# Kernel optimization log

Measured on AMD Instinct MI355X. Metric: run time of the kernel, lower is better.

Reference implementation:

```python
import jax, jax.numpy as jnp
import numpy as np

HEADS = 4
AGENT = 49  # 7x7 agent tokens
LN_EPS = 1e-5


def setup_inputs() -> dict:
    key = jax.random.key(0)
    ks = jax.random.split(key, 3)
    B, C, H, W = 2, 128, 56, 56
    x = jax.random.normal(ks[0], (B, C, H, W), jnp.float32)
    # 1x1 convs == per-pixel linear maps; store as [out_ch, in_ch]
    w_qkv = jax.random.normal(ks[1], (3 * C, C), jnp.float32) * (C ** -0.5)
    w_proj = jax.random.normal(ks[2], (C, C), jnp.float32) * (C ** -0.5)
    b_proj = jnp.zeros((C,), jnp.float32)
    ln_g = jnp.ones((C,), jnp.float32)
    ln_b = jnp.zeros((C,), jnp.float32)
    return {"x": x, "w_qkv": w_qkv, "w_proj": w_proj, "b_proj": b_proj,
            "ln_g": ln_g, "ln_b": ln_b}


def reference(x, w_qkv, w_proj, b_proj, ln_g, ln_b):
    B, C, H, W = x.shape
    heads = HEADS
    hd = C // heads
    N = H * W
    scale = hd ** -0.5
    a = int(AGENT ** 0.5)  # 7; H,W divisible by a -> exact adaptive avg pool

    # 1x1-conv QKV: [B,3C,H,W] -> [B,3,heads,hd,N] -> q,k,v [B,h,N,hd]
    qkv = jnp.einsum('oc,bchw->bohw', w_qkv, x).reshape(B, 3, heads, hd, N)
    q = jnp.transpose(qkv[:, 0], (0, 1, 3, 2))
    k = jnp.transpose(qkv[:, 1], (0, 1, 3, 2))
    v = jnp.transpose(qkv[:, 2], (0, 1, 3, 2))

    # agent tokens: adaptive avg pool to (a,a) == uniform block mean
    agent = x.reshape(B, C, a, H // a, a, W // a).mean(axis=(3, 5))  # [B,C,a,a]
    agent = agent.reshape(B, heads, hd, AGENT)
    agent = jnp.transpose(agent, (0, 1, 3, 2))  # [B,h,A,hd]

    # stage 1: compress q through agent tokens
    q_to_agent = jax.nn.softmax(
        jnp.einsum('bhnd,bhad->bhna', q * scale, agent), axis=-1)  # [B,h,N,A]
    q_compressed = jnp.einsum('bhna,bhad->bhnd', q_to_agent, agent)  # [B,h,N,hd]

    # stage 2: full N x N attention with compressed queries
    attn = jax.nn.softmax(
        jnp.einsum('bhnd,bhmd->bhnm', q_compressed * scale, k), axis=-1)
    out = jnp.einsum('bhnm,bhmd->bhnd', attn, v)  # [B,h,N,hd]

    # merge heads -> [B,N,C], 1x1-conv proj, LayerNorm over C
    out = jnp.transpose(out, (0, 2, 1, 3)).reshape(B, N, C)
    out = jnp.einsum('bnc,oc->bno', out, w_proj) + b_proj
    mu = out.mean(-1, keepdims=True)
    var = out.var(-1, keepdims=True)
    out = (out - mu) / jnp.sqrt(var + LN_EPS) * ln_g + ln_b
    return jnp.transpose(out.reshape(B, H, W, C), (0, 3, 1, 2))
```

## Files before the change

### kernel.cpp

```cpp
#include <hip/hip_runtime.h>
#include <hip/hip_bf16.h>
#include <stdint.h>

typedef unsigned short u16;
typedef __attribute__((ext_vector_type(8))) short short8;
typedef __attribute__((ext_vector_type(4))) short short4v;
typedef __attribute__((ext_vector_type(4))) float f32x4;

#define NB 2
#define NC 128
#define NHD 4
#define HD 32
#define NN 3136
#define NA 49
#define NSPLIT 4
#define NKP 3200
#define NTILE 25
#define SCALE 0.17677669529663687f
#define LOG2E 1.4426950408889634f
#define QSC (SCALE * LOG2E)

__device__ inline u16 bfb(float f) {
    __hip_bfloat16 h = __float2bfloat16(f);
    return *(u16*)&h;
}
__device__ inline float b2f(u16 w) {
    return __uint_as_float(((uint32_t)w) << 16);
}
__device__ inline short4v pack4(float a, float b, float c, float d) {
    union { short4v s; __hip_bfloat162 h[2]; } u;
    u.h[0] = __float22bfloat162_rn(make_float2(a, b));
    u.h[1] = __float22bfloat162_rn(make_float2(c, d));
    return u.s;
}
__device__ inline float ldf(const void* p, size_t i, int f) {
    return f ? b2f(((const u16*)p)[i]) : ((const float*)p)[i];
}
__device__ inline void gld16(const u16* g, u16* l) {
    __builtin_amdgcn_global_load_lds(
        (__attribute__((address_space(1))) void*)(g),
        (__attribute__((address_space(3))) void*)(l), 16, 0, 0);
}
__device__ inline void stage8k(const u16* g, u16* lds, int w, int lane) {
    gld16(g + (size_t)(w * 64 + lane) * 8,       lds + (size_t)w * 512);
    gld16(g + (size_t)(256 + w * 64 + lane) * 8, lds + 2048 + (size_t)w * 512);
}

__global__ void k_detect(const u16* __restrict__ raw, int* __restrict__ flag) {
    __shared__ int cnt;
    if (threadIdx.x == 0) cnt = 0;
    __syncthreads();
    u16 w = raw[threadIdx.x * 97];
    float f = b2f(w);
    float a = fabsf(f);
    if (a >= 1e-4f && a <= 100.0f) atomicAdd(&cnt, 1);
    __syncthreads();
    if (threadIdx.x == 0) *flag = (cnt >= 230) ? 1 : 0;
}

__global__ __launch_bounds__(256) void k_prep(const void* __restrict__ xr,
                                              const void* __restrict__ wq,
                                              const void* __restrict__ wp,
                                              const void* __restrict__ bp,
                                              const void* __restrict__ g,
                                              const void* __restrict__ bb,
                                              u16* __restrict__ xT,
                                              u16* __restrict__ wbf,
                                              u16* __restrict__ wpb,
                                              float* __restrict__ bgb,
                                              u16* __restrict__ agb,
                                              u16* __restrict__ agT,
                                              const int* __restrict__ flag) {
    __shared__ u16 tile[128][18];
    int bx = blockIdx.x, t = threadIdx.x;
    int f = *flag;
    if (bx < 392) {
        int b = bx / 196;
        int n0 = (bx % 196) * 16;
        int c = t >> 1, nh = (t & 1) * 8;
        size_t src = ((size_t)(b * 128 + c)) * NN + n0 + nh;
#pragma unroll
        for (int i = 0; i < 8; ++i) tile[c][nh + i] = bfb(ldf(xr, src + i, f));
        __syncthreads();
        int n = t >> 4, c0 = (t & 15) * 8;
        short8 o;
#pragma unroll
        for (int i = 0; i < 8; ++i) o[i] = (short)tile[c0 + i][n];
        *(short8*)&xT[((size_t)b * NN + n0 + n) * 128 + c0] = o;
    } else if (bx < 584) {
        int i = (bx - 392) * 256 + t;
        wbf[i] = bfb(ldf(wq, i, f));
    } else if (bx < 648) {
        int i = (bx - 584) * 256 + t;
        wpb[i] = bfb(ldf(wp, i, f));
    } else if (bx < 650) {
        int i = (bx - 648) * 256 + t;
        if (i < 128)      bgb[i] = ldf(bp, i, f);
        else if (i < 256) bgb[i] = ldf(g, i - 128, f);
        else if (i < 384) bgb[i] = ldf(bb, i - 256, f);
    } else {
        int idx = (bx - 650) * 256 + t;
        const int NPOOL = NB * NC * NA;
        if (idx < NPOOL) {
            int b = idx / (NC * NA);
            int r = idx % (NC * NA);
            int c = r / NA;
            int a = r % NA;
            int ai = a / 7, aj = a % 7;
            size_t base = ((size_t)(b * NC + c)) * NN + ai * 8 * 56 + aj * 8;
            float s = 0.f;
            if (f) {
                const u16* xp = (const u16*)xr + base;
#pragma unroll
                for (int uu = 0; uu < 8; ++uu) {
                    ushort4 a0 = *(const ushort4*)&xp[uu * 56];
                    ushort4 a1 = *(const ushort4*)&xp[uu * 56 + 4];
                    s += b2f(a0.x) + b2f(a0.y) + b2f(a0.z) + b2f(a0.w)
                       + b2f(a1.x) + b2f(a1.y) + b2f(a1.z) + b2f(a1.w);
                }
            } else {
                const float* xp = (const float*)xr + base;
#pragma unroll
                for (int uu = 0; uu < 8; ++uu) {
                    float4 v0 = *(const float4*)&xp[uu * 56];
                    float4 v1 = *(const float4*)&xp[uu * 56 + 4];
                    s += v0.x + v0.y + v0.z + v0.w + v1.x + v1.y + v1.z + v1.w;
                }
            }
            int h = c >> 5, d = c & 31;
            int bh = b * NHD + h;
            u16 val = bfb(s * (1.f / 64.f));
            agb[bh * 2048 + a * 32 + d] = val;
            agT[bh * 2048 + d * 64 + a] = val;
        } else {
            int j = idx - NPOOL;
            if (j < 3840) {
                int bh = j / 480, rem = j % 480;
                int a = 49 + rem / 32, d = rem % 32;
                agb[bh * 2048 + a * 32 + d] = 0;
            } else if (j < 7680) {
                j -= 3840;
                int bh = j / 480, rem = j % 480;
                int a = 49 + rem / 32, d = rem % 32;
                agT[bh * 2048 + d * 64 + a] = 0;
            }
        }
    }
}

__global__ __launch_bounds__(256, 4) void k_qkv2(const u16* __restrict__ xT,
                                                 const u16* __restrict__ wbf,
                                                 u16* __restrict__ qb,
                                                 u16* __restrict__ kbf,
                                                 u16* __restrict__ vtb) {
    int b = blockIdx.z;
    int n0 = blockIdx.x * 64;
    int w = threadIdx.x >> 6, lane = threadIdx.x & 63;
    int c = lane & 15, u = lane >> 4;
    int o0 = blockIdx.y * 64 + w * 16;
    const f32x4 z = {0.f, 0.f, 0.f, 0.f};
    short8 af0 = *(const short8*)&wbf[(o0 + c) * 128 +  0 + u * 8];
    short8 af1 = *(const short8*)&wbf[(o0 + c) * 128 + 32 + u * 8];
    short8 af2 = *(const short8*)&wbf[(o0 + c) * 128 + 64 + u * 8];
    short8 af3 = *(const short8*)&wbf[(o0 + c) * 128 + 96 + u * 8];
    int tq = o0 >> 7, h = (o0 >> 5) & 3, d0 = (o0 & 31) + u * 4;
    size_t bh = (size_t)b * NHD + h;
    const u16* xb = &xT[(size_t)b * NN * 128];
#pragma unroll
    for (int nt = 0; nt < 4; ++nt) {
        int n = n0 + nt * 16 + c;
        f32x4 acc = z;
        acc = __builtin_amdgcn_mfma_f32_16x16x32_bf16(af0,
            *(const short8*)&xb[(size_t)n * 128 +  0 + u * 8], acc, 0, 0, 0);
        acc = __builtin_amdgcn_mfma_f32_16x16x32_bf16(af1,
            *(const short8*)&xb[(size_t)n * 128 + 32 + u * 8], acc, 0, 0, 0);
        acc = __builtin_amdgcn_mfma_f32_16x16x32_bf16(af2,
            *(const short8*)&xb[(size_t)n * 128 + 64 + u * 8], acc, 0, 0, 0);
        acc = __builtin_amdgcn_mfma_f32_16x16x32_bf16(af3,
            *(const short8*)&xb[(size_t)n * 128 + 96 + u * 8], acc, 0, 0, 0);
        if (tq == 0) {
            *(short4v*)&qb[(bh * NN + n) * HD + d0] =
                pack4(acc[0] * QSC, acc[1] * QSC, acc[2] * QSC, acc[3] * QSC);
        } else if (tq == 1) {
            *(short4v*)&kbf[(bh * NKP + n) * HD + d0] =
                pack4(acc[0], acc[1], acc[2], acc[3]);
        } else {
            int tile = n >> 7, kt2 = n & 127;
            int sub = kt2 >> 4, uu = (kt2 >> 2) & 3, jj = n & 3;
            size_t vb0 = ((size_t)bh * NTILE + tile) * 4096 + sub * 512 + uu * 128 + jj;
#pragma unroll
            for (int r = 0; r < 4; ++r)
                vtb[vb0 + (d0 + r) * 4] = bfb(acc[r]);
        }
    }
}

__global__ __launch_bounds__(256, 4) void k_stage1_2(const u16* __restrict__ qb,
                                                     const u16* __restrict__ agb,
                                                     const u16* __restrict__ agT,
                                                     u16* __restrict__ qcb) {
    int b = blockIdx.z, h = blockIdx.y;
    int w = threadIdx.x >> 6, lane = threadIdx.x & 63;
    int c = lane & 15, u = lane >> 4;
    int q0 = blockIdx.x * 64 + w * 16;
    size_t bh = (size_t)b * NHD + h;
    const u16* aB = agb + bh * 2048;
    const u16* aT = agT + bh * 2048;
    const f32x4 z = {0.f, 0.f, 0.f, 0.f};
    short8 qf = *(const short8*)&qb[(bh * NN + q0 + c) * HD + u * 8];
    f32x4 st[4];
#pragma unroll
    for (int t = 0; t < 4; ++t) {
        short8 afr = *(const short8*)&aB[(t * 16 + c) * 32 + u * 8];
        st[t] = __builtin_amdgcn_mfma_f32_16x16x32_bf16(afr, qf, z, 0, 0, 0);
    }
    float e[4][4];
    float lsum = 0.f;
#pragma unroll
    for (int t = 0; t < 4; ++t)
#pragma unroll
        for (int r = 0; r < 4; ++r) {
            float v = __builtin_amdgcn_exp2f(st[t][r]);
            if (t == 3 && !(u == 0 && r == 0)) v = 0.f;
            e[t][r] = v;
            lsum += v;
        }
    lsum += __shfl_xor(lsum, 16);
    lsum += __shfl_xor(lsum, 32);
    float linv = 1.f / lsum;
    f32x4 qlo = z, qhi = z;
#pragma unroll
    for (int t = 0; t < 4; ++t) {
        short4v pf = pack4(e[t][0] * linv, e[t][1] * linv, e[t][2] * linv, e[t][3] * linv);
        short4v alo = *(const short4v*)&aT[c * 64 + t * 16 + u * 4];
        short4v ahi = *(const short4v*)&aT[(c + 16) * 64 + t * 16 + u * 4];
        qlo = __builtin_amdgcn_mfma_f32_16x16x16bf16_1k(alo, pf, qlo, 0, 0, 0);
        qhi = __builtin_amdgcn_mfma_f32_16x16x16bf16_1k(ahi, pf, qhi, 0, 0, 0);
    }
    u16* dst = &qcb[(bh * NN + q0 + c) * HD];
    *(short4v*)&dst[u * 4]      = pack4(qlo[0] * QSC, qlo[1] * QSC, qlo[2] * QSC, qlo[3] * QSC);
    *(short4v*)&dst[16 + u * 4] = pack4(qhi[0] * QSC, qhi[1] * QSC, qhi[2] * QSC, qhi[3] * QSC);
}

__global__ __launch_bounds__(256, 3) void k_flash4(const u16* __restrict__ qc,
                                                   const u16* __restrict__ kb,
                                                   const u16* __restrict__ vt,
                                                   float* __restrict__ op,
                                                   float* __restrict__ lp) {
    __shared__ __align__(16) u16 Ks[2][4096];
    __shared__ __align__(16) u16 Vs[2][4096];
    int b = blockIdx.z;
    int h = blockIdx.y & 3;
    int s = blockIdx.y >> 2;
    int w = threadIdx.x >> 6, lane = threadIdx.x & 63;
    int c = lane & 15, u = lane >> 4;
    int qa = blockIdx.x * 128 + w * 32;
    int qbr = qa + 16;
    if (qa  > NN - 16) qa  = NN - 16;
    if (qbr > NN - 16) qbr = NN - 16;
    size_t bh = (size_t)b * NHD + h;
    const u16* kg = kb + bh * (size_t)NKP * HD;
    const u16* vg = vt + bh * (size_t)NTILE * 4096;
    short8 qfA = *(const short8*)(qc + (bh * NN + qa  + c) * HD + u * 8);
    short8 qfB = *(const short8*)(qc + (bh * NN + qbr + c) * HD + u * 8);
    const f32x4 z = {0.f, 0.f, 0.f, 0.f};
    f32x4 oA0 = z, oA1 = z, oB0 = z, oB1 = z;
    float lA = 0.f, lB = 0.f;
    int t0 = (s * NTILE) / NSPLIT, t1 = ((s + 1) * NTILE) / NSPLIT;
    stage8k(kg + (size_t)t0 * 4096, &Ks[0][0], w, lane);
    stage8k(vg + (size_t)t0 * 4096, &Vs[0][0], w, lane);
#pragma unroll 1
    for (int t = t0; t < t1; ++t) {
        int buf = (t - t0) & 1;
        __syncthreads();
        if (t + 1 < t1) {
            stage8k(kg + (size_t)(t + 1) * 4096, &Ks[buf ^ 1][0], w, lane);
            stage8k(vg + (size_t)(t + 1) * 4096, &Vs[buf ^ 1][0], w, lane);
        }
        const u16* kp = &Ks[buf][0];
        const u16* vp = &Vs[buf][0];
        int kk = t * 128;
        bool tail = (kk + 128 > NN);
#pragma unroll
        for (int sub = 0; sub < 8; ++sub) {
            short8 kf = *(const short8*)(kp + sub * 512 + c * 32 + u * 8);
            f32x4 sA = __builtin_amdgcn_mfma_f32_16x16x32_bf16(kf, qfA, z, 0, 0, 0);
            f32x4 sB = __builtin_amdgcn_mfma_f32_16x16x32_bf16(kf, qfB, z, 0, 0, 0);
            float eA[4], eB[4];
#pragma unroll
            for (int r = 0; r < 4; ++r) {
                eA[r] = __builtin_amdgcn_exp2f(sA[r]);
                eB[r] = __builtin_amdgcn_exp2f(sB[r]);
            }
            if (tail) {
#pragma unroll
                for (int r = 0; r < 4; ++r)
                    if (kk + sub * 16 + u * 4 + r >= NN) { eA[r] = 0.f; eB[r] = 0.f; }
            }
            lA += (eA[0] + eA[1]) + (eA[2] + eA[3]);
            lB += (eB[0] + eB[1]) + (eB[2] + eB[3]);
            short4v pA = pack4(eA[0], eA[1], eA[2], eA[3]);
            short4v pB = pack4(eB[0], eB[1], eB[2], eB[3]);
            short4v va = *(const short4v*)(vp + sub * 512 + u * 128 + c * 4);
            short4v vb = *(const short4v*)(vp + sub * 512 + u * 128 + (c + 16) * 4);
            oA0 = __builtin_amdgcn_mfma_f32_16x16x16bf16_1k(va, pA, oA0, 0, 0, 0);
            oA1 = __builtin_amdgcn_mfma_f32_16x16x16bf16_1k(vb, pA, oA1, 0, 0, 0);
            oB0 = __builtin_amdgcn_mfma_f32_16x16x16bf16_1k(va, pB, oB0, 0, 0, 0);
            oB1 = __builtin_amdgcn_mfma_f32_16x16x16bf16_1k(vb, pB, oB1, 0, 0, 0);
        }
    }
    lA += __shfl_xor(lA, 16); lA += __shfl_xor(lA, 32);
    lB += __shfl_xor(lB, 16); lB += __shfl_xor(lB, 32);
    float* oba = op + (((size_t)(s * NB + b)) * NN + qa + c) * NC + h * HD;
    *(f32x4*)&oba[u * 4]      = oA0;
    *(f32x4*)&oba[16 + u * 4] = oA1;
    float* obb = op + (((size_t)(s * NB + b)) * NN + qbr + c) * NC + h * HD;
    *(f32x4*)&obb[u * 4]      = oB0;
    *(f32x4*)&obb[16 + u * 4] = oB1;
    if (u == 0) {
        lp[(((size_t)(s * NB + b)) * NHD + h) * NN + qa  + c] = lA;
        lp[(((size_t)(s * NB + b)) * NHD + h) * NN + qbr + c] = lB;
    }
}

__global__ __launch_bounds__(256, 4) void k_proj2(const float* __restrict__ op,
                                                  const float* __restrict__ lp,
                                                  const u16* __restrict__ wpb,
                                                  const float* __restrict__ bgb,
                                                  void* __restrict__ out,
                                                  const int* __restrict__ flag) {
    __shared__ u16 Af[16 * 136];
    __shared__ float red1[4][16], red2[4][16];
    int bx = blockIdx.x;
    int b = bx >= 196;
    int n0 = (bx - b * 196) * 16;
    int t = threadIdx.x;
    {
        int row = t >> 4, c8 = (t & 15) * 8;
        int n = n0 + row;
        int hh = c8 >> 5;
        float ls = 0.f;
#pragma unroll
        for (int s = 0; s < NSPLIT; ++s)
            ls += lp[(((size_t)(s * NB + b)) * NHD + hh) * NN + n];
        float inv = 1.f / ls;
        float v[8] = {};
#pragma unroll
        for (int s = 0; s < NSPLIT; ++s) {
            const float* src = &op[(((size_t)(s * NB + b)) * NN + n) * NC + c8];
            float4 x0 = *(const float4*)&src[0];
            float4 x1 = *(const float4*)&src[4];
            v[0] += x0.x; v[1] += x0.y; v[2] += x0.z; v[3] += x0.w;
            v[4] += x1.x; v[5] += x1.y; v[6] += x1.z; v[7] += x1.w;
        }
        u16* dst = &Af[row * 136 + c8];
#pragma unroll
        for (int i = 0; i < 8; i += 2) {
            __hip_bfloat162 p = __float22bfloat162_rn(make_float2(v[i] * inv, v[i + 1] * inv));
            *(uint32_t*)&dst[i] = *(uint32_t*)&p;
        }
    }
    __syncthreads();
    int w = t >> 6, lane = t & 63, c = lane & 15, u = lane >> 4;
    int oA = w * 32 + c, oB = w * 32 + 16 + c;
    const f32x4 z = {0.f, 0.f, 0.f, 0.f};
    f32x4 cA = z, cB = z;
#pragma unroll
    for (int kf = 0; kf < 4; ++kf) {
        short8 a  = *(const short8*)&Af[c * 136 + kf * 32 + u * 8];
        short8 bA = *(const short8*)&wpb[(size_t)oA * 128 + kf * 32 + u * 8];
        short8 bB = *(const short8*)&wpb[(size_t)oB * 128 + kf * 32 + u * 8];
        cA = __builtin_amdgcn_mfma_f32_16x16x32_bf16(a, bA, cA, 0, 0, 0);
        cB = __builtin_amdgcn_mfma_f32_16x16x32_bf16(a, bB, cB, 0, 0, 0);
    }
    float bpA = bgb[oA], bpB = bgb[oB];
    float s1[4], s2[4];
#pragma unroll
    for (int r = 0; r < 4; ++r) {
        cA[r] += bpA; cB[r] += bpB;
        s1[r] = cA[r] + cB[r];
        s2[r] = cA[r] * cA[r] + cB[r] * cB[r];
    }
#pragma unroll
    for (int off = 1; off < 16; off <<= 1)
#pragma unroll
        for (int r = 0; r < 4; ++r) {
            s1[r] += __shfl_xor(s1[r], off);
            s2[r] += __shfl_xor(s2[r], off);
        }
    if (c == 0)
#pragma unroll
        for (int r = 0; r < 4; ++r) {
            red1[w][u * 4 + r] = s1[r];
            red2[w][u * 4 + r] = s2[r];
        }
    __syncthreads();
    float gA = bgb[128 + oA], beA = bgb[256 + oA];
    float gB = bgb[128 + oB], beB = bgb[256 + oB];
    float outA[4], outB[4];
#pragma unroll
    for (int r = 0; r < 4; ++r) {
        int row = u * 4 + r;
        float S1 = (red1[0][row] + red1[1][row]) + (red1[2][row] + red1[3][row]);
        float S2 = (red2[0][row] + red2[1][row]) + (red2[2][row] + red2[3][row]);
        float mu = S1 * (1.f / NC);
        float ex = S2 * (1.f / NC);
        float rstd = rsqrtf(ex - mu * mu + 1e-5f);
        outA[r] = (cA[r] - mu) * rstd * gA + beA;
        outB[r] = (cB[r] - mu) * rstd * gB + beB;
    }
    int n = n0 + u * 4;
    if (*flag) {
        __hip_bfloat16* ob = (__hip_bfloat16*)out;
        ushort4 sA = make_ushort4(bfb(outA[0]), bfb(outA[1]), bfb(outA[2]), bfb(outA[3]));
        ushort4 sB = make_ushort4(bfb(outB[0]), bfb(outB[1]), bfb(outB[2]), bfb(outB[3]));
        *(ushort4*)&ob[((size_t)(b * NC + oA)) * NN + n] = sA;
        *(ushort4*)&ob[((size_t)(b * NC + oB)) * NN + n] = sB;
    } else {
        float* ob = (float*)out;
        *(float4*)&ob[((size_t)(b * NC + oA)) * NN + n] = make_float4(outA[0], outA[1], outA[2], outA[3]);
        *(float4*)&ob[((size_t)(b * NC + oB)) * NN + n] = make_float4(outB[0], outB[1], outB[2], outB[3]);
    }
}

extern "C" void kernel_launch(void* const* d_in, const int* in_sizes, int n_in,
                              void* d_out, int out_size, void* d_ws, size_t ws_size,
                              hipStream_t stream) {
    const void* x_raw  = d_in[0];
    const void* wq_raw = d_in[1];
    const void* wp_raw = d_in[2];
    const void* bp_raw = d_in[3];
    const void* lg_raw = d_in[4];
    const void* lb_raw = d_in[5];

    float* ws   = (float*)d_ws;
    int*   flag = (int*)d_ws;
    float* bgb  = ws + 16;
    float* op   = bgb + 512;
    float* lp   = op + (size_t)NSPLIT * NB * NN * NC;
    u16*   xT   = (u16*)(lp + (size_t)NSPLIT * NB * NHD * NN);
    u16*   wbf  = xT + (size_t)NB * NN * NC;
    u16*   wpb  = wbf + 3 * NC * NC;
    u16*   qb   = wpb + NC * NC;
    u16*   kbf  = qb + (size_t)NB * NHD * NN * HD;
    u16*   vtb  = kbf + (size_t)NB * NHD * NKP * HD;
    u16*   qcb  = vtb + (size_t)NB * NHD * NTILE * 4096;
    u16*   agb  = qcb + (size_t)NB * NHD * NN * HD;
    u16*   agT  = agb + NB * NHD * 64 * 32;

    k_detect<<<1, 256, 0, stream>>>((const u16*)x_raw, flag);
    k_prep<<<729, 256, 0, stream>>>(x_raw, wq_raw, wp_raw, bp_raw, lg_raw, lb_raw,
                                    xT, wbf, wpb, bgb, agb, agT, flag);
    k_qkv2<<<dim3(NN / 64, 6, NB), 256, 0, stream>>>(xT, wbf, qb, kbf, vtb);
    k_stage1_2<<<dim3(NN / 64, NHD, NB), 256, 0, stream>>>(qb, agb, agT, qcb);
    k_flash4<<<dim3(25, NHD * NSPLIT, NB), 256, 0, stream>>>(qcb, kbf, vtb, op, lp);
    k_proj2<<<392, 256, 0, stream>>>(op, lp, wpb, bgb, d_out, flag);
}
```

Measured before the change: 124.0 us.

## Fuse detect into prep, stage1 into QKV, and store flash partials as bf16

Each prep block now runs the dtype detection itself, which removes the separate detect launch. The agent-compression stage now runs inside the QKV kernel on a Q tile kept in shared memory, so Q is never written to or read back from global memory and one more launch goes away. Flash partial outputs are normalised and stored as bf16 instead of fp32, which halves the traffic into the projection kernel; that kernel recombines the splits weighted by their sums. The cost is some lost precision in the partials and a serial stage1 tail in only two of the six y-blocks of the QKV grid.

```diff
diff --git a/kernel.cpp b/kernel.cpp
--- a/kernel.cpp
+++ b/kernel.cpp
@@ -45,17 +45,14 @@
     gld16(g + (size_t)(w * 64 + lane) * 8,       lds + (size_t)w * 512);
     gld16(g + (size_t)(256 + w * 64 + lane) * 8, lds + 2048 + (size_t)w * 512);
 }
-
-__global__ void k_detect(const u16* __restrict__ raw, int* __restrict__ flag) {
+__device__ inline int detect_local(const u16* raw, int t) {
     __shared__ int cnt;
-    if (threadIdx.x == 0) cnt = 0;
+    if (t == 0) cnt = 0;
     __syncthreads();
-    u16 w = raw[threadIdx.x * 97];
-    float f = b2f(w);
-    float a = fabsf(f);
+    float a = fabsf(b2f(raw[t * 97]));
     if (a >= 1e-4f && a <= 100.0f) atomicAdd(&cnt, 1);
     __syncthreads();
-    if (threadIdx.x == 0) *flag = (cnt >= 230) ? 1 : 0;
+    return cnt >= 230;
 }
 
 __global__ __launch_bounds__(256) void k_prep(const void* __restrict__ xr,
@@ -70,10 +67,10 @@
                                               float* __restrict__ bgb,
                                               u16* __restrict__ agb,
                                               u16* __restrict__ agT,
-                                              const int* __restrict__ flag) {
+                                              int* __restrict__ flagOut) {
     __shared__ u16 tile[128][18];
     int bx = blockIdx.x, t = threadIdx.x;
-    int f = *flag;
+    int f = detect_local((const u16*)xr, t);
     if (bx < 392) {
         int b = bx / 196;
         int n0 = (bx % 196) * 16;
@@ -98,6 +95,7 @@
         if (i < 128)      bgb[i] = ldf(bp, i, f);
         else if (i < 256) bgb[i] = ldf(g, i - 128, f);
         else if (i < 384) bgb[i] = ldf(bb, i - 256, f);
+        if (bx == 648 && t == 0) *flagOut = f;
     } else {
         int idx = (bx - 650) * 256 + t;
         const int NPOOL = NB * NC * NA;
@@ -148,11 +146,14 @@
     }
 }
 
-__global__ __launch_bounds__(256, 4) void k_qkv2(const u16* __restrict__ xT,
-                                                 const u16* __restrict__ wbf,
-                                                 u16* __restrict__ qb,
-                                                 u16* __restrict__ kbf,
-                                                 u16* __restrict__ vtb) {
+__global__ __launch_bounds__(256, 4) void k_qkv_s1(const u16* __restrict__ xT,
+                                                   const u16* __restrict__ wbf,
+                                                   const u16* __restrict__ agb,
+                                                   const u16* __restrict__ agT,
+                                                   u16* __restrict__ kbf,
+                                                   u16* __restrict__ vtb,
+                                                   u16* __restrict__ qcb) {
+    __shared__ u16 qtile[2 * 64 * 40];
     int b = blockIdx.z;
     int n0 = blockIdx.x * 64;
     int w = threadIdx.x >> 6, lane = threadIdx.x & 63;
@@ -179,7 +180,8 @@
         acc = __builtin_amdgcn_mfma_f32_16x16x32_bf16(af3,
             *(const short8*)&xb[(size_t)n * 128 + 96 + u * 8], acc, 0, 0, 0);
         if (tq == 0) {
-            *(short4v*)&qb[(bh * NN + n) * HD + d0] =
+            int hl = (o0 >> 5) & 1;
+            *(short4v*)&qtile[(hl * 64 + nt * 16 + c) * 40 + d0] =
                 pack4(acc[0] * QSC, acc[1] * QSC, acc[2] * QSC, acc[3] * QSC);
         } else if (tq == 1) {
             *(short4v*)&kbf[(bh * NKP + n) * HD + d0] =
@@ -193,59 +195,57 @@
                 vtb[vb0 + (d0 + r) * 4] = bfb(acc[r]);
         }
     }
-}
-
-__global__ __launch_bounds__(256, 4) void k_stage1_2(const u16* __restrict__ qb,
-                                                     const u16* __restrict__ agb,
-                                                     const u16* __restrict__ agT,
-                                                     u16* __restrict__ qcb) {
-    int b = blockIdx.z, h = blockIdx.y;
-    int w = threadIdx.x >> 6, lane = threadIdx.x & 63;
-    int c = lane & 15, u = lane >> 4;
-    int q0 = blockIdx.x * 64 + w * 16;
-    size_t bh = (size_t)b * NHD + h;
-    const u16* aB = agb + bh * 2048;
-    const u16* aT = agT + bh * 2048;
-    const f32x4 z = {0.f, 0.f, 0.f, 0.f};
-    short8 qf = *(const short8*)&qb[(bh * NN + q0 + c) * HD + u * 8];
-    f32x4 st[4];
-#pragma unroll
-    for (int t = 0; t < 4; ++t) {
-        short8 afr = *(const short8*)&aB[(t * 16 + c) * 32 + u * 8];
-        st[t] = __builtin_amdgcn_mfma_f32_16x16x32_bf16(afr, qf, z, 0, 0, 0);
-    }
-    float e[4][4];
-    float lsum = 0.f;
-#pragma unroll
-    for (int t = 0; t < 4; ++t)
-#pragma unroll
-        for (int r = 0; r < 4; ++r) {
-            float v = __builtin_amdgcn_exp2f(st[t][r]);
-            if (t == 3 && !(u == 0 && r == 0)) v = 0.f;
-            e[t][r] = v;
-            lsum += v;
-        }
-    lsum += __shfl_xor(lsum, 16);
-    lsum += __shfl_xor(lsum, 32);
-    float linv = 1.f / lsum;
-    f32x4 qlo = z, qhi = z;
-#pragma unroll
-    for (int t = 0; t < 4; ++t) {
-        short4v pf = pack4(e[t][0] * linv, e[t][1] * linv, e[t][2] * linv, e[t][3] * linv);
-        short4v alo = *(const short4v*)&aT[c * 64 + t * 16 + u * 4];
-        short4v ahi = *(const short4v*)&aT[(c + 16) * 64 + t * 16 + u * 4];
-        qlo = __builtin_amdgcn_mfma_f32_16x16x16bf16_1k(alo, pf, qlo, 0, 0, 0);
-        qhi = __builtin_amdgcn_mfma_f32_16x16x16bf16_1k(ahi, pf, qhi, 0, 0, 0);
-    }
-    u16* dst = &qcb[(bh * NN + q0 + c) * HD];
-    *(short4v*)&dst[u * 4]      = pack4(qlo[0] * QSC, qlo[1] * QSC, qlo[2] * QSC, qlo[3] * QSC);
-    *(short4v*)&dst[16 + u * 4] = pack4(qhi[0] * QSC, qhi[1] * QSC, qhi[2] * QSC, qhi[3] * QSC);
+    if (blockIdx.y < 2) {
+        __syncthreads();
+#pragma unroll
+        for (int tt = w; tt < 8; tt += 4) {
+            int hl2 = tt >> 2, r0 = (tt & 3) * 16;
+            int hg = blockIdx.y * 2 + hl2;
+            size_t bh2 = (size_t)b * NHD + hg;
+            const u16* aB = agb + bh2 * 2048;
+            const u16* aT = agT + bh2 * 2048;
+            short8 qf = *(const short8*)&qtile[(hl2 * 64 + r0 + c) * 40 + u * 8];
+            f32x4 st[4];
+#pragma unroll
+            for (int t2 = 0; t2 < 4; ++t2) {
+                short8 afr = *(const short8*)&aB[(t2 * 16 + c) * 32 + u * 8];
+                st[t2] = __builtin_amdgcn_mfma_f32_16x16x32_bf16(afr, qf, z, 0, 0, 0);
+            }
+            float e[4][4];
+            float lsum = 0.f;
+#pragma unroll
+            for (int t2 = 0; t2 < 4; ++t2)
+#pragma unroll
+                for (int r = 0; r < 4; ++r) {
+                    float v = __builtin_amdgcn_exp2f(st[t2][r]);
+                    if (t2 == 3 && !(u == 0 && r == 0)) v = 0.f;
+                    e[t2][r] = v;
+                    lsum += v;
+                }
+            lsum += __shfl_xor(lsum, 16);
+            lsum += __shfl_xor(lsum, 32);
+            float linv = 1.f / lsum;
+            f32x4 qlo = z, qhi = z;
+#pragma unroll
+            for (int t2 = 0; t2 < 4; ++t2) {
+                short4v pf = pack4(e[t2][0] * linv, e[t2][1] * linv,
+                                   e[t2][2] * linv, e[t2][3] * linv);
+                short4v alo = *(const short4v*)&aT[c * 64 + t2 * 16 + u * 4];
+                short4v ahi = *(const short4v*)&aT[(c + 16) * 64 + t2 * 16 + u * 4];
+                qlo = __builtin_amdgcn_mfma_f32_16x16x16bf16_1k(alo, pf, qlo, 0, 0, 0);
+                qhi = __builtin_amdgcn_mfma_f32_16x16x16bf16_1k(ahi, pf, qhi, 0, 0, 0);
+            }
+            u16* dst = &qcb[(bh2 * NN + n0 + r0 + c) * HD];
+            *(short4v*)&dst[u * 4]      = pack4(qlo[0] * QSC, qlo[1] * QSC, qlo[2] * QSC, qlo[3] * QSC);
+            *(short4v*)&dst[16 + u * 4] = pack4(qhi[0] * QSC, qhi[1] * QSC, qhi[2] * QSC, qhi[3] * QSC);
+        }
+    }
 }
 
 __global__ __launch_bounds__(256, 3) void k_flash4(const u16* __restrict__ qc,
                                                    const u16* __restrict__ kb,
                                                    const u16* __restrict__ vt,
-                                                   float* __restrict__ op,
+                                                   u16* __restrict__ opb,
                                                    float* __restrict__ lp) {
     __shared__ __align__(16) u16 Ks[2][4096];
     __shared__ __align__(16) u16 Vs[2][4096];
@@ -311,19 +311,20 @@
     }
     lA += __shfl_xor(lA, 16); lA += __shfl_xor(lA, 32);
     lB += __shfl_xor(lB, 16); lB += __shfl_xor(lB, 32);
-    float* oba = op + (((size_t)(s * NB + b)) * NN + qa + c) * NC + h * HD;
-    *(f32x4*)&oba[u * 4]      = oA0;
-    *(f32x4*)&oba[16 + u * 4] = oA1;
-    float* obb = op + (((size_t)(s * NB + b)) * NN + qbr + c) * NC + h * HD;
-    *(f32x4*)&obb[u * 4]      = oB0;
-    *(f32x4*)&obb[16 + u * 4] = oB1;
+    float iA = 1.f / lA, iB = 1.f / lB;
+    u16* oba = opb + (((size_t)(s * NB + b)) * NN + qa + c) * NC + h * HD;
+    *(short4v*)&oba[u * 4]      = pack4(oA0[0] * iA, oA0[1] * iA, oA0[2] * iA, oA0[3] * iA);
+    *(short4v*)&oba[16 + u * 4] = pack4(oA1[0] * iA, oA1[1] * iA, oA1[2] * iA, oA1[3] * iA);
+    u16* obb = opb + (((size_t)(s * NB + b)) * NN + qbr + c) * NC + h * HD;
+    *(short4v*)&obb[u * 4]      = pack4(oB0[0] * iB, oB0[1] * iB, oB0[2] * iB, oB0[3] * iB);
+    *(short4v*)&obb[16 + u * 4] = pack4(oB1[0] * iB, oB1[1] * iB, oB1[2] * iB, oB1[3] * iB);
     if (u == 0) {
         lp[(((size_t)(s * NB + b)) * NHD + h) * NN + qa  + c] = lA;
         lp[(((size_t)(s * NB + b)) * NHD + h) * NN + qbr + c] = lB;
     }
 }
 
-__global__ __launch_bounds__(256, 4) void k_proj2(const float* __restrict__ op,
+__global__ __launch_bounds__(256, 4) void k_proj2(const u16* __restrict__ opb,
                                                   const float* __restrict__ lp,
                                                   const u16* __restrict__ wpb,
                                                   const float* __restrict__ bgb,
@@ -339,24 +340,22 @@
         int row = t >> 4, c8 = (t & 15) * 8;
         int n = n0 + row;
         int hh = c8 >> 5;
-        float ls = 0.f;
-#pragma unroll
-        for (int s = 0; s < NSPLIT; ++s)
-            ls += lp[(((size_t)(s * NB + b)) * NHD + hh) * NN + n];
-        float inv = 1.f / ls;
-        float v[8] = {};
+        float num[8] = {};
+        float den = 0.f;
 #pragma unroll
         for (int s = 0; s < NSPLIT; ++s) {
-            const float* src = &op[(((size_t)(s * NB + b)) * NN + n) * NC + c8];
-            float4 x0 = *(const float4*)&src[0];
-            float4 x1 = *(const float4*)&src[4];
-            v[0] += x0.x; v[1] += x0.y; v[2] += x0.z; v[3] += x0.w;
-            v[4] += x1.x; v[5] += x1.y; v[6] += x1.z; v[7] += x1.w;
-        }
+            float ls = lp[(((size_t)(s * NB + b)) * NHD + hh) * NN + n];
+            short8 o8 = *(const short8*)&opb[(((size_t)(s * NB + b)) * NN + n) * NC + c8];
+            den += ls;
+#pragma unroll
+            for (int i = 0; i < 8; ++i) num[i] += ls * b2f((u16)o8[i]);
+        }
+        float inv = 1.f / den;
         u16* dst = &Af[row * 136 + c8];
 #pragma unroll
         for (int i = 0; i < 8; i += 2) {
-            __hip_bfloat162 p = __float22bfloat162_rn(make_float2(v[i] * inv, v[i + 1] * inv));
+            __hip_bfloat162 p = __float22bfloat162_rn(
+                make_float2(num[i] * inv, num[i + 1] * inv));
             *(uint32_t*)&dst[i] = *(uint32_t*)&p;
         }
     }
@@ -436,23 +435,21 @@
     float* ws   = (float*)d_ws;
     int*   flag = (int*)d_ws;
     float* bgb  = ws + 16;
-    float* op   = bgb + 512;
-    float* lp   = op + (size_t)NSPLIT * NB * NN * NC;
-    u16*   xT   = (u16*)(lp + (size_t)NSPLIT * NB * NHD * NN);
+    float* lp   = bgb + 512;
+    u16*   opb  = (u16*)(lp + (size_t)NSPLIT * NB * NHD * NN);
+    u16*   xT   = opb + (size_t)NSPLIT * NB * NN * NC;
     u16*   wbf  = xT + (size_t)NB * NN * NC;
     u16*   wpb  = wbf + 3 * NC * NC;
-    u16*   qb   = wpb + NC * NC;
-    u16*   kbf  = qb + (size_t)NB * NHD * NN * HD;
+    u16*   kbf  = wpb + NC * NC;
     u16*   vtb  = kbf + (size_t)NB * NHD * NKP * HD;
     u16*   qcb  = vtb + (size_t)NB * NHD * NTILE * 4096;
     u16*   agb  = qcb + (size_t)NB * NHD * NN * HD;
     u16*   agT  = agb + NB * NHD * 64 * 32;
 
-    k_detect<<<1, 256, 0, stream>>>((const u16*)x_raw, flag);
     k_prep<<<729, 256, 0, stream>>>(x_raw, wq_raw, wp_raw, bp_raw, lg_raw, lb_raw,
                                     xT, wbf, wpb, bgb, agb, agT, flag);
-    k_qkv2<<<dim3(NN / 64, 6, NB), 256, 0, stream>>>(xT, wbf, qb, kbf, vtb);
-    k_stage1_2<<<dim3(NN / 64, NHD, NB), 256, 0, stream>>>(qb, agb, agT, qcb);
-    k_flash4<<<dim3(25, NHD * NSPLIT, NB), 256, 0, stream>>>(qcb, kbf, vtb, op, lp);
-    k_proj2<<<392, 256, 0, stream>>>(op, lp, wpb, bgb, d_out, flag);
-}
+    k_qkv_s1<<<dim3(NN / 64, 6, NB), 256, 0, stream>>>(xT, wbf, agb, agT,
+                                                       kbf, vtb, qcb);
+    k_flash4<<<dim3(25, NHD * NSPLIT, NB), 256, 0, stream>>>(qcb, kbf, vtb, opb, lp);
+    k_proj2<<<392, 256, 0, stream>>>(opb, lp, wpb, bgb, d_out, flag);
+}
```

Measured after the change: 119.3 us. -3.8%, faster.
